# Optimization experiments

Hardware: AMD Instinct MI355X
Metric: run time of the kernel (lower is better)

## Reference

```python
import jax, jax.numpy as jnp
import numpy as np

PI = float(np.pi)
SIGMA = 1.0          # density_smearing_width
NUM_GRAPHS = 16
K_TOTAL = 16384
N_NODES = 4096


def setup_inputs() -> dict:
    key = jax.random.key(0)
    k1, k2, k3, k4, k5, k6 = jax.random.split(key, 6)
    k_vectors = jax.random.normal(k1, (K_TOTAL, 3), jnp.float32) * 2.0
    k_norm2 = jnp.sum(k_vectors * k_vectors, axis=-1)            # [K]
    k_vector_batch = jnp.sort(jax.random.randint(k2, (K_TOTAL,), 0, NUM_GRAPHS, dtype=jnp.int32))
    k0_mask = jnp.zeros((K_TOTAL,), jnp.float32)                 # no k=0 vectors
    source_feats = jax.random.normal(k3, (N_NODES, 1), jnp.float32)   # monopole charges (max_l=0)
    node_positions = jax.random.normal(k4, (N_NODES, 3), jnp.float32) * 3.0
    batch = jnp.sort(jax.random.randint(k5, (N_NODES,), 0, NUM_GRAPHS, dtype=jnp.int32))
    volume = jax.random.uniform(k6, (NUM_GRAPHS,), jnp.float32, minval=100.0, maxval=300.0)
    pbc = jnp.ones((NUM_GRAPHS, 3), dtype=bool)
    return {"k_vectors": k_vectors, "k_norm2": k_norm2, "k_vector_batch": k_vector_batch,
            "k0_mask": k0_mask, "source_feats": source_feats, "node_positions": node_positions,
            "batch": batch, "volume": volume, "pbc": pbc}


def reference(k_vectors, k_norm2, k_vector_batch, k0_mask, source_feats,
              node_positions, batch, volume, pbc):
    # pbc is all-True -> static PBC (reciprocal-space) branch.
    B = volume.shape[0]
    # [K, N] phase matrix, masked to block-diagonal (same-graph) structure
    inner = k_vectors @ node_positions.T
    mask_f = (k_vector_batch[:, None] == batch[None, :]).astype(inner.dtype)
    cosines = jnp.cos(inner) * mask_f
    sines = jnp.sin(inner) * mask_f
    # GTO (Gaussian, max_l=0) density basis Fourier transform
    fs = jnp.exp(-0.5 * (SIGMA ** 2) * k_norm2)                  # [K]
    q = source_feats[:, 0]                                       # [N] monopole coeffs
    vol_per_k = volume[k_vector_batch]                           # [K]
    pref = fs * (2.0 * PI) ** 3 / vol_per_k                      # [K]
    # assemble_fourier_series_batch: real/imag structure factors
    density = jnp.stack([cosines @ q, sines @ q], axis=-1) * pref[:, None]   # [K, 2]
    # Coulomb kernel 4*pi/k^2, zeroed at k=0
    k0_bool = k0_mask > 0.0
    k_factor = jnp.where(k0_bool, 0.0, 1.0 / jnp.where(k0_bool, 1.0, k_norm2))
    potential = 4.0 * PI * density * k_factor[:, None]           # [K, 2]
    # energy_product_batch: segment-reduce per-k energies to graphs
    per_k = 2.0 * jnp.sum(density * potential, axis=-1)          # [K]
    energy_k = jax.ops.segment_sum(per_k, k_vector_batch, num_segments=B)
    energy = 0.5 * volume * energy_k / (2.0 * PI) ** 6           # [B]
    # subtract Gaussian self-interaction (include_self_interaction=False)
    self_fields = q / (SIGMA * jnp.sqrt(2.0 * PI))
    node_energies = q * self_fields
    self_energy = jax.ops.segment_sum(node_energies, batch, num_segments=B)
    return energy - 0.5 * self_energy
```

## Files before the change

### kernel.cpp

```cpp
#include <hip/hip_runtime.h>
#include <math.h>

#define NUM_GRAPHS 16
#define PI_F 3.14159265358979323846f
#define INV_SQRT_2PI 0.3989422804014327f

__global__ void gto_init_kernel(const float* __restrict__ q,
                                const int* __restrict__ batch, int n_nodes,
                                float* __restrict__ out,
                                int* __restrict__ node_start ) {
    __shared__ float acc[NUM_GRAPHS];
    int t = threadIdx.x;
    if (t < NUM_GRAPHS) acc[t] = 0.f;
    __syncthreads();

    if (t <= NUM_GRAPHS) {
        int lo = 0, hi = n_nodes;
        while (lo < hi) {
            int mid = (lo + hi) >> 1;
            if (batch[mid] < t) lo = mid + 1; else hi = mid;
        }
        node_start[t] = lo;
    }

    for (int i = t; i < n_nodes; i += blockDim.x) {
        float qi = q[i];
        atomicAdd(&acc[batch[i]], qi * qi);
    }
    __syncthreads();
    if (t < NUM_GRAPHS) {
        out[t] = -0.5f * acc[t] * INV_SQRT_2PI;
    }
}

#define WAVES_PER_BLOCK 4
#define K_PER_WAVE 8
#define K_PER_BLOCK (WAVES_PER_BLOCK * K_PER_WAVE)

__global__ void __launch_bounds__(256)
gto_energy_kernel(const float* __restrict__ kvec,
                  const float* __restrict__ knorm2,
                  const int*   __restrict__ kbatch,
                  const float* __restrict__ k0mask,
                  const float* __restrict__ q,
                  const float* __restrict__ pos,
                  const float* __restrict__ volume,
                  const int*   __restrict__ node_start,
                  float* __restrict__ out, int K) {
    __shared__ float gacc[NUM_GRAPHS];
    int t = threadIdx.x;
    if (t < NUM_GRAPHS) gacc[t] = 0.f;
    __syncthreads();

    int wave = t >> 6;
    int lane = t & 63;
    int kbase = (blockIdx.x * WAVES_PER_BLOCK + wave) * K_PER_WAVE;

    for (int kk = 0; kk < K_PER_WAVE; ++kk) {
        int k = kbase + kk;
        if (k >= K) break;
        int g = kbatch[k];
        float kx = kvec[3 * k + 0];
        float ky = kvec[3 * k + 1];
        float kz = kvec[3 * k + 2];
        int s = node_start[g];
        int e = node_start[g + 1];

        float C = 0.f, S = 0.f;
        for (int j = s + lane; j < e; j += 64) {
            float px = pos[3 * j + 0];
            float py = pos[3 * j + 1];
            float pz = pos[3 * j + 2];
            float inner = fmaf(kx, px, fmaf(ky, py, kz * pz));
            float sv, cv;
            __sincosf(inner, &sv, &cv);
            float qj = q[j];
            C = fmaf(cv, qj, C);
            S = fmaf(sv, qj, S);
        }
        #pragma unroll
        for (int off = 32; off > 0; off >>= 1) {
            C += __shfl_xor(C, off, 64);
            S += __shfl_xor(S, off, 64);
        }
        if (lane == 0) {
            float kn2 = knorm2[k];
            float fs = __expf(-0.5f * kn2);
            float kfac = (k0mask[k] > 0.f) ? 0.f : 1.f / kn2;
            float e_k = 4.f * PI_F * kfac * fs * fs * (C * C + S * S) / volume[g];
            atomicAdd(&gacc[g], e_k);
        }
    }
    __syncthreads();
    if (t < NUM_GRAPHS && gacc[t] != 0.f) {
        atomicAdd(&out[t], gacc[t]);
    }
}

extern "C" void kernel_launch(void* const* d_in, const int* in_sizes, int n_in,
                              void* d_out, int out_size, void* d_ws, size_t ws_size,
                              hipStream_t stream) {
    const float* k_vectors  = (const float*)d_in[0];
    const float* k_norm2    = (const float*)d_in[1];
    const int*   k_batch    = (const int*)  d_in[2];
    const float* k0_mask    = (const float*)d_in[3];
    const float* src_feats  = (const float*)d_in[4];
    const float* positions  = (const float*)d_in[5];
    const int*   batch      = (const int*)  d_in[6];
    const float* volume     = (const float*)d_in[7];

    int K = in_sizes[1];
    int N = in_sizes[4];
    float* out = (float*)d_out;
    int* node_start = (int*)d_ws;

    gto_init_kernel<<<1, 256, 0, stream>>>(src_feats, batch, N, out, node_start);

    int blocks = (K + K_PER_BLOCK - 1) / K_PER_BLOCK;
    gto_energy_kernel<<<blocks, 256, 0, stream>>>(
        k_vectors, k_norm2, k_batch, k0_mask, src_feats, positions,
        volume, node_start, out, K);
}
```

Measured before the change: 92.10 us.

## Remap energy lanes to 16 k-vectors per wave and rewrite init segment scan

The energy kernel now gives each wave 16 k-vectors at once, with 4 lanes per k splitting that graph's nodes. This replaces 8 sequential k-vectors per wave, each needing a full 64-lane shuffle reduction, and cuts the reduction to two shuffle steps. The init kernel finds graph boundaries by comparing neighbouring batch entries instead of binary search. It then reduces the per-graph self-energy with one wave per graph instead of contended shared-memory atomics. In exchange each lane runs a longer serial node loop, the grid has half as many blocks, and k-vectors in one wave that belong to different graphs can make the loop diverge.

```diff
diff --git a/kernel.cpp b/kernel.cpp
--- a/kernel.cpp
+++ b/kernel.cpp
@@ -5,37 +5,50 @@
 #define PI_F 3.14159265358979323846f
 #define INV_SQRT_2PI 0.3989422804014327f
 
-__global__ void gto_init_kernel(const float* __restrict__ q,
-                                const int* __restrict__ batch, int n_nodes,
-                                float* __restrict__ out,
-                                int* __restrict__ node_start ) {
-    __shared__ float acc[NUM_GRAPHS];
+__global__ void __launch_bounds__(256)
+gto_init_kernel(const float* __restrict__ q,
+                const int* __restrict__ batch, int n_nodes,
+                float* __restrict__ out,
+                int* __restrict__ node_start ) {
+    __shared__ int ns[NUM_GRAPHS + 1];
     int t = threadIdx.x;
-    if (t < NUM_GRAPHS) acc[t] = 0.f;
+
+    if (t == 0) {
+        ns[0] = 0;
+        int bl = batch[n_nodes - 1];
+        for (int g = bl + 1; g <= NUM_GRAPHS; ++g) ns[g] = n_nodes;
+    }
     __syncthreads();
 
-    if (t <= NUM_GRAPHS) {
-        int lo = 0, hi = n_nodes;
-        while (lo < hi) {
-            int mid = (lo + hi) >> 1;
-            if (batch[mid] < t) lo = mid + 1; else hi = mid;
+    for (int i = t; i < n_nodes - 1; i += 256) {
+        int b0 = batch[i];
+        int b1 = batch[i + 1];
+        if (b0 != b1) {
+            for (int g = b0 + 1; g <= b1; ++g) ns[g] = i + 1;
         }
-        node_start[t] = lo;
+    }
+    __syncthreads();
+
+    int wave = t >> 6;
+    int lane = t & 63;
+    for (int g = wave; g < NUM_GRAPHS; g += 4) {
+        int s = ns[g], e = ns[g + 1];
+        float acc = 0.f;
+        for (int j = s + lane; j < e; j += 64) {
+            float qj = q[j];
+            acc = fmaf(qj, qj, acc);
+        }
+        #pragma unroll
+        for (int off = 32; off > 0; off >>= 1) acc += __shfl_xor(acc, off, 64);
+        if (lane == 0) out[g] = -0.5f * acc * INV_SQRT_2PI;
     }
 
-    for (int i = t; i < n_nodes; i += blockDim.x) {
-        float qi = q[i];
-        atomicAdd(&acc[batch[i]], qi * qi);
-    }
-    __syncthreads();
-    if (t < NUM_GRAPHS) {
-        out[t] = -0.5f * acc[t] * INV_SQRT_2PI;
-    }
+    if (t <= NUM_GRAPHS) node_start[t] = ns[t];
 }
 
+#define K_PER_WAVE 16
 #define WAVES_PER_BLOCK 4
-#define K_PER_WAVE 8
-#define K_PER_BLOCK (WAVES_PER_BLOCK * K_PER_WAVE)
+#define K_PER_BLOCK (K_PER_WAVE * WAVES_PER_BLOCK)
 
 __global__ void __launch_bounds__(256)
 gto_energy_kernel(const float* __restrict__ kvec,
@@ -54,11 +67,11 @@
 
     int wave = t >> 6;
     int lane = t & 63;
-    int kbase = (blockIdx.x * WAVES_PER_BLOCK + wave) * K_PER_WAVE;
+    int ksub = lane & 15;
+    int noff = lane >> 4;
 
-    for (int kk = 0; kk < K_PER_WAVE; ++kk) {
-        int k = kbase + kk;
-        if (k >= K) break;
+    int k = (blockIdx.x * WAVES_PER_BLOCK + wave) * K_PER_WAVE + ksub;
+    if (k < K) {
         int g = kbatch[k];
         float kx = kvec[3 * k + 0];
         float ky = kvec[3 * k + 1];
@@ -67,7 +80,7 @@
         int e = node_start[g + 1];
 
         float C = 0.f, S = 0.f;
-        for (int j = s + lane; j < e; j += 64) {
+        for (int j = s + noff; j < e; j += 4) {
             float px = pos[3 * j + 0];
             float py = pos[3 * j + 1];
             float pz = pos[3 * j + 2];
@@ -78,12 +91,12 @@
             C = fmaf(cv, qj, C);
             S = fmaf(sv, qj, S);
         }
-        #pragma unroll
-        for (int off = 32; off > 0; off >>= 1) {
-            C += __shfl_xor(C, off, 64);
-            S += __shfl_xor(S, off, 64);
-        }
-        if (lane == 0) {
+        C += __shfl_xor(C, 16, 64);
+        S += __shfl_xor(S, 16, 64);
+        C += __shfl_xor(C, 32, 64);
+        S += __shfl_xor(S, 32, 64);
+
+        if (noff == 0) {
             float kn2 = knorm2[k];
             float fs = __expf(-0.5f * kn2);
             float kfac = (k0mask[k] > 0.f) ? 0.f : 1.f / kn2;
```

Result: slower. 95.30 us (+3.5%).
